# Optimization experiments

Measured on AMD Instinct MI355X. Metric: run time of the kernel, lower is better.

## Reference

```python
import jax, jax.numpy as jnp
import numpy as np

B, S, K, N = 4, 2048, 4096, 11008


def setup_inputs() -> dict:
    key = jax.random.key(0)
    k_x, k_w, k_s, k_z, k_b = jax.random.split(key, 5)
    x = jax.random.normal(k_x, (B, S, K), dtype=jnp.float32)
    qweight = jax.random.randint(k_w, (N, K), 0, 256, dtype=jnp.int32)
    scale = jax.random.uniform(k_s, (N, 1), dtype=jnp.float32) * 0.01 + 1e-4
    zero_point = jax.random.uniform(k_z, (N, 1), dtype=jnp.float32) * 255.0
    bias = jax.random.normal(k_b, (N,), dtype=jnp.float32)
    return {"x": x, "qweight": qweight, "scale": scale, "zero_point": zero_point, "bias": bias}


def reference(x, qweight, scale, zero_point, bias):
    # Dequantize int8 weights per output channel (group_size=-1):
    # w[n, k] = (qweight[n, k] - zero_point[n]) * scale[n]
    w = (qweight.astype(jnp.float32) - zero_point) * scale  # [N, K]
    # Fused dequant-matmul + bias: y = x @ w.T + b
    y = jnp.einsum('bsk,nk->bsn', x, w) + bias  # [B, S, N]
    return y
```

## Files before the change

### kernel.cpp

```cpp
#include <hip/hip_runtime.h>
#include <hip/hip_bf16.h>
#include <stdint.h>

#define M_DIM 8192
#define N_DIM 11008
#define K_DIM 4096
#define NTILE 64

typedef unsigned short ushort_t;
typedef __attribute__((ext_vector_type(8)))  short  short8;
typedef __attribute__((ext_vector_type(8)))  __bf16 bf16x8;
typedef __attribute__((ext_vector_type(4)))  float  f32x4;
typedef __attribute__((ext_vector_type(4)))  int    i32x4;
typedef __attribute__((ext_vector_type(16))) char   char16;

__device__ __forceinline__ ushort_t f2bf(float f){
  uint32_t u = __builtin_bit_cast(uint32_t, f);
  u += 0x7FFFu + ((u >> 16) & 1u);
  return (ushort_t)(u >> 16);
}

__device__ __forceinline__ void gll16(const void* g, void* l){
  __builtin_amdgcn_global_load_lds(
      (const __attribute__((address_space(1))) void*)g,
      (__attribute__((address_space(3))) void*)l,
      16, 0, 0);
}

__global__ __launch_bounds__(256)
void quant_x(const float* __restrict__ x, signed char* __restrict__ xq,
             float* __restrict__ sxv, float* __restrict__ sxs){
  const int row  = blockIdx.x;
  const int t    = threadIdx.x;
  const int lane = t & 63, wid = t >> 6;
  const float* xr = x + (size_t)row * K_DIM;

  float e[16];
  {
    const float4* p = (const float4*)(xr + t*16);
    float4 v0 = p[0], v1 = p[1], v2 = p[2], v3 = p[3];
    e[0]=v0.x; e[1]=v0.y; e[2]=v0.z; e[3]=v0.w;
    e[4]=v1.x; e[5]=v1.y; e[6]=v1.z; e[7]=v1.w;
    e[8]=v2.x; e[9]=v2.y; e[10]=v2.z; e[11]=v2.w;
    e[12]=v3.x; e[13]=v3.y; e[14]=v3.z; e[15]=v3.w;
  }
  float am = 0.f;
  #pragma unroll
  for (int j=0;j<16;++j) am = fmaxf(am, fabsf(e[j]));
  #pragma unroll
  for (int off=32; off; off>>=1) am = fmaxf(am, __shfl_xor(am, off));

  __shared__ float sm[4];
  __shared__ float ss[4];
  if (lane == 0) sm[wid] = am;
  __syncthreads();
  const float amax = fmaxf(fmaxf(sm[0],sm[1]), fmaxf(sm[2],sm[3]));
  const float inv = amax > 0.f ? 127.f/amax : 0.f;
  const float sx  = amax > 0.f ? amax*(1.f/127.f) : 1.f;

  char16 c;
  float fs = 0.f;
  #pragma unroll
  for (int j=0;j<16;++j){
    float r = rintf(e[j]*inv);
    fs += r;
    c[j] = (signed char)(int)r;
  }
  *(char16*)(xq + (size_t)row*K_DIM + t*16) = c;

  #pragma unroll
  for (int off=32; off; off>>=1) fs += __shfl_xor(fs, off);
  if (lane == 0) ss[wid] = fs;
  __syncthreads();
  if (t == 0){
    sxv[row] = sx;
    sxs[row] = ss[0]+ss[1]+ss[2]+ss[3];
  }
}

__global__ void cvt_w8(const int* __restrict__ q, signed char* __restrict__ wq){
  const int TOT = (int)((size_t)N_DIM*K_DIM/16);
  for (int c = blockIdx.x*blockDim.x + threadIdx.x; c < TOT; c += gridDim.x*blockDim.x){
    size_t i = (size_t)c*16;
    int4 a = *(const int4*)(q+i);
    int4 b = *(const int4*)(q+i+4);
    int4 d = *(const int4*)(q+i+8);
    int4 f = *(const int4*)(q+i+12);
    char16 o;
    o[0]=(signed char)(a.x-128);  o[1]=(signed char)(a.y-128);
    o[2]=(signed char)(a.z-128);  o[3]=(signed char)(a.w-128);
    o[4]=(signed char)(b.x-128);  o[5]=(signed char)(b.y-128);
    o[6]=(signed char)(b.z-128);  o[7]=(signed char)(b.w-128);
    o[8]=(signed char)(d.x-128);  o[9]=(signed char)(d.y-128);
    o[10]=(signed char)(d.z-128); o[11]=(signed char)(d.w-128);
    o[12]=(signed char)(f.x-128); o[13]=(signed char)(f.y-128);
    o[14]=(signed char)(f.z-128); o[15]=(signed char)(f.w-128);
    *(char16*)(wq+i) = o;
  }
}


#define BAR() do{ asm volatile("" ::: "memory"); \
  __builtin_amdgcn_s_barrier(); \
  asm volatile("" ::: "memory"); }while(0)

#define LGKM0() asm volatile("s_waitcnt lgkmcnt(0)" ::: "memory")

#define VMW2() do{ __builtin_amdgcn_sched_barrier(0); \
  asm volatile("s_waitcnt vmcnt(2)" ::: "memory"); \
  __builtin_amdgcn_sched_barrier(0); }while(0)

#define VMW0() do{ __builtin_amdgcn_sched_barrier(0); \
  asm volatile("s_waitcnt vmcnt(0)" ::: "memory"); \
  __builtin_amdgcn_sched_barrier(0); }while(0)

#define LDA_TO(DST, BUF, G) do{ \
  const signed char* _b = &As[BUF][wm][0]; \
  _Pragma("unroll") for (int mf=0; mf<4; ++mf) \
    DST[mf] = *(const i32x4*)(_b + ((G)*64 + mf*16 + rl)*64 + offk); \
}while(0)

#define LDB_TO(DST, BUF, NG) do{ \
  const signed char* _b = &Bs[BUF][hb][0]; \
  _Pragma("unroll") for (int nfl=0; nfl<2; ++nfl) \
    DST[nfl] = *(const i32x4*)(_b + (hbr + (NG)*32 + nfl*16 + rl)*64 + offk); \
}while(0)

#define MM_Q(AF, BF, MG, NG) do{ \
  __builtin_amdgcn_s_setprio(1); \
  _Pragma("unroll") for (int mf=0; mf<4; ++mf) \
    _Pragma("unroll") for (int nfl=0; nfl<2; ++nfl) \
      acc[(MG)*4+mf][(NG)*2+nfl] = __builtin_amdgcn_mfma_i32_16x16x64_i8( \
          AF[mf], BF[nfl], acc[(MG)*4+mf][(NG)*2+nfl], 0, 0, 0); \
  __builtin_amdgcn_s_setprio(0); \
}while(0)

#define STAGE_A(BUF, H, T) gll16(aS[H] + (size_t)(T)*64, &As[BUF][H][w*1024])
#define STAGE_B(BUF, H, T) gll16(bS[H] + (size_t)(T)*64, &Bs[BUF][H][w*1024])

__global__ __launch_bounds__(512, 1)
void qgemm256_i8(const signed char* __restrict__ Xq, const signed char* __restrict__ Wq,
                 const float* __restrict__ g_scale, const float* __restrict__ g_zp,
                 const float* __restrict__ g_bias,
                 const float* __restrict__ sxv, const float* __restrict__ sxs,
                 float* __restrict__ Y)
{
  __shared__ __align__(16) signed char As[2][2][8192];
  __shared__ __align__(16) signed char Bs[2][2][8192];

  const int t    = threadIdx.x;
  const int lane = t & 63;
  const int w    = t >> 6;
  const int wm   = w >> 2;
  const int wn   = w & 3;
  const int hb   = wn >> 1;
  const int hbr  = (wn & 1) * 64;

  const int GM2 = M_DIM/256, GN2 = N_DIM/256;
  const int NWG2 = GM2*GN2;
  int bid = blockIdx.x;
  int swz = (bid & 7) * (NWG2/8) + (bid >> 3);
  int by = swz / GN2, bx = swz - by*GN2;
  const int brow = by*256, bcol = bx*256;

  const int rl   = lane & 15;
  const int offk = ((lane >> 4) ^ ((rl >> 1) & 3)) * 16;

  const int g_s = (lane & 3) ^ ((lane >> 3) & 3);
  const signed char* aS[2];
  const signed char* bS[2];
  #pragma unroll
  for (int h=0; h<2; ++h){
    int r = h*128 + w*16 + (lane >> 2);
    aS[h] = Xq + (size_t)(brow + r)*K_DIM + g_s*16;
    bS[h] = Wq + (size_t)(bcol + r)*K_DIM + g_s*16;
  }

  i32x4 acc[8][4] = {};
  i32x4 afX[4], afY[4];
  i32x4 bfX[2], bfY[2];

  STAGE_B(0,0,0); STAGE_A(0,0,0); STAGE_A(0,1,0); STAGE_B(0,1,0);
  STAGE_B(1,0,1); STAGE_A(1,0,1);
  VMW2();
  BAR();

  #pragma unroll 1
  for (int j=0; j<NTILE/2-1; ++j){
    const int t1 = 2*j+1, t2 = 2*j+2, t3 = 2*j+3;
    LDA_TO(afX, 0, 0);
    LDB_TO(bfX, 0, 0);
    STAGE_A(1,1,t1);
    BAR(); LGKM0();
    MM_Q(afX, bfX, 0, 0);
    BAR();
    LDB_TO(bfY, 0, 1);
    STAGE_B(1,1,t1);
    BAR(); LGKM0();
    MM_Q(afX, bfY, 0, 1);
    BAR();
    LDA_TO(afY, 0, 1);
    STAGE_B(0,0,t2);
    BAR(); LGKM0();
    MM_Q(afY, bfX, 1, 0);
    BAR();
    STAGE_A(0,0,t2);
    VMW2();
    BAR();
    MM_Q(afY, bfY, 1, 1);
    BAR();
    LDA_TO(afX, 1, 0);
    LDB_TO(bfX, 1, 0);
    STAGE_A(0,1,t2);
    BAR(); LGKM0();
    MM_Q(afX, bfX, 0, 0);
    BAR();
    LDB_TO(bfY, 1, 1);
    STAGE_B(0,1,t2);
    BAR(); LGKM0();
    MM_Q(afX, bfY, 0, 1);
    BAR();
    LDA_TO(afY, 1, 1);
    STAGE_B(1,0,t3);
    BAR(); LGKM0();
    MM_Q(afY, bfX, 1, 0);
    BAR();
    STAGE_A(1,0,t3);
    VMW2();
    BAR();
    MM_Q(afY, bfY, 1, 1);
    BAR();
  }

  {
    const int t1 = NTILE-1;
    LDA_TO(afX, 0, 0);
    LDB_TO(bfX, 0, 0);
    STAGE_A(1,1,t1);
    BAR(); LGKM0();
    MM_Q(afX, bfX, 0, 0);
    BAR();
    LDB_TO(bfY, 0, 1);
    STAGE_B(1,1,t1);
    BAR(); LGKM0();
    MM_Q(afX, bfY, 0, 1);
    BAR();
    LDA_TO(afY, 0, 1);
    BAR(); LGKM0();
    MM_Q(afY, bfX, 1, 0);
    BAR();
    VMW0();
    BAR();
    MM_Q(afY, bfY, 1, 1);
    BAR();
    LDA_TO(afX, 1, 0);
    LDB_TO(bfX, 1, 0);
    BAR(); LGKM0();
    MM_Q(afX, bfX, 0, 0);
    BAR();
    LDB_TO(bfY, 1, 1);
    BAR(); LGKM0();
    MM_Q(afX, bfY, 0, 1);
    BAR();
    LDA_TO(afY, 1, 1);
    BAR(); LGKM0();
    MM_Q(afY, bfX, 1, 0);
    BAR();
    MM_Q(afY, bfY, 1, 1);
  }

  const int cl = lane & 15;
  const int rq = (lane >> 4) << 2;
  float sN[4], cN[4], bN[4];
  #pragma unroll
  for (int nf=0; nf<4; ++nf){
    int col = bcol + wn*64 + nf*16 + cl;
    float s = g_scale[col];
    sN[nf] = s;
    cN[nf] = s * (128.f - g_zp[col]);
    bN[nf] = g_bias[col];
  }
  #pragma unroll
  for (int mf=0; mf<8; ++mf){
    const int rowb = brow + wm*128 + mf*16 + rq;
    float sx0 = sxv[rowb],   sx1 = sxv[rowb+1], sx2 = sxv[rowb+2], sx3 = sxv[rowb+3];
    float t0 = sx0*sxs[rowb],   t1 = sx1*sxs[rowb+1];
    float t2 = sx2*sxs[rowb+2], t3 = sx3*sxs[rowb+3];
    #pragma unroll
    for (int nf=0; nf<4; ++nf){
      int col = bcol + wn*64 + nf*16 + cl;
      size_t base = (size_t)rowb*N_DIM + col;
      i32x4 v = acc[mf][nf];
      Y[base            ] = (float)v[0]*(sN[nf]*sx0) + t0*cN[nf] + bN[nf];
      Y[base +   N_DIM  ] = (float)v[1]*(sN[nf]*sx1) + t1*cN[nf] + bN[nf];
      Y[base + 2*N_DIM  ] = (float)v[2]*(sN[nf]*sx2) + t2*cN[nf] + bN[nf];
      Y[base + 3*N_DIM  ] = (float)v[3]*(sN[nf]*sx3) + t3*cN[nf] + bN[nf];
    }
  }
}

__global__ __launch_bounds__(256, 2)
void qgemm_fb(const float* __restrict__ Xf, const int* __restrict__ Wq,
              const float* __restrict__ g_scale, const float* __restrict__ g_zp,
              const float* __restrict__ g_bias, float* __restrict__ Y)
{
  const int BM=128, BK=64, NT=K_DIM/BK, GRID_N=N_DIM/128, NWG=(M_DIM/128)*GRID_N;
  __shared__ __align__(16) ushort_t As[2][BM*BK];
  __shared__ __align__(16) ushort_t Bs[2][BM*BK];

  const int t = threadIdx.x, lane = t & 63, w = t >> 6;
  const int wr = w >> 1, wc = w & 1;
  int bid = blockIdx.x;
  int swz = (bid & 7) * (NWG/8) + (bid >> 3);
  int by = swz / GRID_N, bx = swz - by*GRID_N;
  const int brow = by*128, bcol = bx*128;

  f32x4 acc[4][4] = {};
  const int s8 = t & 7, r0 = t >> 3;

  float wsc[4], wof[4];
  #pragma unroll
  for (int i=0;i<4;++i){
    int n = bcol + r0 + 32*i;
    float sc = g_scale[n];
    wsc[i] = sc; wof[i] = -g_zp[n]*sc;
  }
  float4 ax[4][2]; int4 bq[4][2];
  auto loadA = [&](int kt){
    #pragma unroll
    for (int i=0;i<4;++i){
      const float* p = Xf + (size_t)(brow + r0 + 32*i)*K_DIM + kt*BK + s8*8;
      ax[i][0] = *(const float4*)p; ax[i][1] = *(const float4*)(p+4);
    }};
  auto loadB = [&](int kt){
    #pragma unroll
    for (int i=0;i<4;++i){
      const int* p = Wq + (size_t)(bcol + r0 + 32*i)*K_DIM + kt*BK + s8*8;
      bq[i][0] = *(const int4*)p; bq[i][1] = *(const int4*)(p+4);
    }};
  auto stageA = [&](int buf){
    #pragma unroll
    for (int i=0;i<4;++i){
      short8 o;
      o[0]=(short)f2bf(ax[i][0].x); o[1]=(short)f2bf(ax[i][0].y);
      o[2]=(short)f2bf(ax[i][0].z); o[3]=(short)f2bf(ax[i][0].w);
      o[4]=(short)f2bf(ax[i][1].x); o[5]=(short)f2bf(ax[i][1].y);
      o[6]=(short)f2bf(ax[i][1].z); o[7]=(short)f2bf(ax[i][1].w);
      int r = r0 + 32*i; int idx = (r*BK + s8*8) ^ ((r&7)<<3);
      *(short8*)&As[buf][idx] = o; }};
  auto stageB = [&](int buf){
    #pragma unroll
    for (int i=0;i<4;++i){
      short8 o;
      o[0]=(short)f2bf((float)bq[i][0].x*wsc[i]+wof[i]);
      o[1]=(short)f2bf((float)bq[i][0].y*wsc[i]+wof[i]);
      o[2]=(short)f2bf((float)bq[i][0].z*wsc[i]+wof[i]);
      o[3]=(short)f2bf((float)bq[i][0].w*wsc[i]+wof[i]);
      o[4]=(short)f2bf((float)bq[i][1].x*wsc[i]+wof[i]);
      o[5]=(short)f2bf((float)bq[i][1].y*wsc[i]+wof[i]);
      o[6]=(short)f2bf((float)bq[i][1].z*wsc[i]+wof[i]);
      o[7]=(short)f2bf((float)bq[i][1].w*wsc[i]+wof[i]);
      int r = r0 + 32*i; int idx = (r*BK + s8*8) ^ ((r&7)<<3);
      *(short8*)&Bs[buf][idx] = o; }};

  loadA(0); loadB(0);
  stageA(0); stageB(0);
  if (NT > 1){ loadA(1); loadB(1); }

  int cur = 0;
  for (int kt=0; kt<NT; ++kt){
    asm volatile("s_waitcnt vmcnt(0) lgkmcnt(0)" ::: "memory");
    __builtin_amdgcn_sched_barrier(0);
    __syncthreads();
    const int nxt = cur ^ 1;
    if (kt+1 < NT){
      stageA(nxt); stageB(nxt);
      if (kt+2 < NT){ loadA(kt+2); loadB(kt+2); }
    }
    const ushort_t* as = As[cur];
    const ushort_t* bs = Bs[cur];
    #pragma unroll
    for (int kk=0; kk<2; ++kk){
      bf16x8 af[4], bfr[4];
      const int klo = kk*32 + ((lane>>4)<<3);
      #pragma unroll
      for (int mf=0; mf<4; ++mf){
        int r = wr*64 + mf*16 + (lane&15);
        af[mf] = *(const bf16x8*)&as[(r*BK + klo) ^ ((r&7)<<3)];
      }
      #pragma unroll
      for (int nf=0; nf<4; ++nf){
        int r = wc*64 + nf*16 + (lane&15);
        bfr[nf] = *(const bf16x8*)&bs[(r*BK + klo) ^ ((r&7)<<3)];
      }
      #pragma unroll
      for (int mf=0; mf<4; ++mf)
        #pragma unroll
        for (int nf=0; nf<4; ++nf)
          acc[mf][nf] = __builtin_amdgcn_mfma_f32_16x16x32_bf16(af[mf], bfr[nf], acc[mf][nf], 0,0,0);
    }
    cur = nxt;
  }
  const int cl = lane & 15, rq = (lane >> 4) << 2;
  #pragma unroll
  for (int nf=0; nf<4; ++nf){
    int col = bcol + wc*64 + nf*16 + cl;
    float bvs = g_bias[col];
    #pragma unroll
    for (int mf=0; mf<4; ++mf){
      int row = brow + wr*64 + mf*16 + rq;
      f32x4 v = acc[mf][nf];
      #pragma unroll
      for (int i=0;i<4;++i)
        Y[(size_t)(row+i)*N_DIM + col] = v[i] + bvs;
    }
  }
}

extern "C" void kernel_launch(void* const* d_in, const int* in_sizes, int n_in,
                              void* d_out, int out_size, void* d_ws, size_t ws_size,
                              hipStream_t stream) {
  const float* x     = (const float*)d_in[0];
  const int*   qw    = (const int*)  d_in[1];
  const float* scale = (const float*)d_in[2];
  const float* zp    = (const float*)d_in[3];
  const float* bias  = (const float*)d_in[4];
  float* y = (float*)d_out;

  const size_t XQ = (size_t)M_DIM*K_DIM;
  const size_t WQ = (size_t)N_DIM*K_DIM;
  const size_t SV = (size_t)M_DIM*4;
  const size_t need = XQ + WQ + 2*SV;

  if (ws_size >= need){
    signed char* xq = (signed char*)d_ws;
    signed char* wq = (signed char*)d_ws + XQ;
    float* sxv = (float*)((char*)d_ws + XQ + WQ);
    float* sxs = sxv + M_DIM;
    quant_x<<<dim3(M_DIM), dim3(256), 0, stream>>>(x, xq, sxv, sxs);
    cvt_w8<<<dim3(2048), dim3(256), 0, stream>>>(qw, wq);
    qgemm256_i8<<<dim3((M_DIM/256)*(N_DIM/256)), dim3(512), 0, stream>>>(
        xq, wq, scale, zp, bias, sxv, sxs, y);
  } else {
    qgemm_fb<<<dim3((M_DIM/128)*(N_DIM/128)), dim3(256), 0, stream>>>(
        x, qw, scale, zp, bias, y);
  }
}
```

Before: 572.3 us.

## Prefetch LDS fragments one phase ahead with partial lgkmcnt waits

```diff
diff --git a/kernel.cpp b/kernel.cpp
--- a/kernel.cpp
+++ b/kernel.cpp
@@ -104,7 +104,9 @@
   __builtin_amdgcn_s_barrier(); \
   asm volatile("" ::: "memory"); }while(0)
 
-#define LGKM0() asm volatile("s_waitcnt lgkmcnt(0)" ::: "memory")
+#define LGKMW(N) do{ \
+  asm volatile("s_waitcnt lgkmcnt(" #N ")" ::: "memory"); \
+  __builtin_amdgcn_sched_barrier(0); }while(0)
 
 #define VMW2() do{ __builtin_amdgcn_sched_barrier(0); \
   asm volatile("s_waitcnt vmcnt(2)" ::: "memory"); \
@@ -184,88 +186,104 @@
   STAGE_B(1,0,1); STAGE_A(1,0,1);
   VMW2();
   BAR();
+  LDA_TO(afX, 0, 0);
+  LDB_TO(bfX, 0, 0);
 
   #pragma unroll 1
   for (int j=0; j<NTILE/2-1; ++j){
     const int t1 = 2*j+1, t2 = 2*j+2, t3 = 2*j+3;
+    LDB_TO(bfY, 0, 1);
+    STAGE_A(1,1,t1);
+    BAR();
+    LGKMW(2);
+    MM_Q(afX, bfX, 0, 0);
+    BAR();
+    LDA_TO(afY, 0, 1);
+    STAGE_B(1,1,t1);
+    BAR();
+    LGKMW(4);
+    MM_Q(afX, bfY, 0, 1);
+    BAR();
+    STAGE_B(0,0,t2);
+    BAR();
+    LGKMW(0);
+    MM_Q(afY, bfX, 1, 0);
+    BAR();
+    STAGE_A(0,0,t2);
+    VMW2();
+    BAR();
+    LDA_TO(afX, 1, 0);
+    LDB_TO(bfX, 1, 0);
+    LGKMW(6);
+    MM_Q(afY, bfY, 1, 1);
+    BAR();
+    LDB_TO(bfY, 1, 1);
+    STAGE_A(0,1,t2);
+    BAR();
+    LGKMW(2);
+    MM_Q(afX, bfX, 0, 0);
+    BAR();
+    LDA_TO(afY, 1, 1);
+    STAGE_B(0,1,t2);
+    BAR();
+    LGKMW(4);
+    MM_Q(afX, bfY, 0, 1);
+    BAR();
+    STAGE_B(1,0,t3);
+    BAR();
+    LGKMW(0);
+    MM_Q(afY, bfX, 1, 0);
+    BAR();
+    STAGE_A(1,0,t3);
+    VMW2();
+    BAR();
     LDA_TO(afX, 0, 0);
     LDB_TO(bfX, 0, 0);
+    LGKMW(6);
+    MM_Q(afY, bfY, 1, 1);
+    BAR();
+  }
+
+  {
+    const int t1 = NTILE-1;
+    LDB_TO(bfY, 0, 1);
     STAGE_A(1,1,t1);
-    BAR(); LGKM0();
+    BAR();
+    LGKMW(2);
     MM_Q(afX, bfX, 0, 0);
     BAR();
-    LDB_TO(bfY, 0, 1);
+    LDA_TO(afY, 0, 1);
     STAGE_B(1,1,t1);
-    BAR(); LGKM0();
+    BAR();
+    LGKMW(4);
     MM_Q(afX, bfY, 0, 1);
     BAR();
-    LDA_TO(afY, 0, 1);
-    STAGE_B(0,0,t2);
-    BAR(); LGKM0();
+    BAR();
+    LGKMW(0);
     MM_Q(afY, bfX, 1, 0);
     BAR();
-    STAGE_A(0,0,t2);
-    VMW2();
-    BAR();
-    MM_Q(afY, bfY, 1, 1);
+    VMW0();
     BAR();
     LDA_TO(afX, 1, 0);
     LDB_TO(bfX, 1, 0);
-    STAGE_A(0,1,t2);
-    BAR(); LGKM0();
+    LGKMW(6);
+    MM_Q(afY, bfY, 1, 1);
+    BAR();
+    LDB_TO(bfY, 1, 1);
+    BAR();
+    LGKMW(2);
     MM_Q(afX, bfX, 0, 0);
     BAR();
-    LDB_TO(bfY, 1, 1);
-    STAGE_B(0,1,t2);
-    BAR(); LGKM0();
+    LDA_TO(afY, 1, 1);
+    BAR();
+    LGKMW(4);
     MM_Q(afX, bfY, 0, 1);
     BAR();
-    LDA_TO(afY, 1, 1);
-    STAGE_B(1,0,t3);
-    BAR(); LGKM0();
+    BAR();
+    LGKMW(0);
     MM_Q(afY, bfX, 1, 0);
     BAR();
-    STAGE_A(1,0,t3);
-    VMW2();
-    BAR();
-    MM_Q(afY, bfY, 1, 1);
-    BAR();
-  }
-
-  {
-    const int t1 = NTILE-1;
-    LDA_TO(afX, 0, 0);
-    LDB_TO(bfX, 0, 0);
-    STAGE_A(1,1,t1);
-    BAR(); LGKM0();
-    MM_Q(afX, bfX, 0, 0);
-    BAR();
-    LDB_TO(bfY, 0, 1);
-    STAGE_B(1,1,t1);
-    BAR(); LGKM0();
-    MM_Q(afX, bfY, 0, 1);
-    BAR();
-    LDA_TO(afY, 0, 1);
-    BAR(); LGKM0();
-    MM_Q(afY, bfX, 1, 0);
-    BAR();
-    VMW0();
-    BAR();
-    MM_Q(afY, bfY, 1, 1);
-    BAR();
-    LDA_TO(afX, 1, 0);
-    LDB_TO(bfX, 1, 0);
-    BAR(); LGKM0();
-    MM_Q(afX, bfX, 0, 0);
-    BAR();
-    LDB_TO(bfY, 1, 1);
-    BAR(); LGKM0();
-    MM_Q(afX, bfY, 0, 1);
-    BAR();
-    LDA_TO(afY, 1, 1);
-    BAR(); LGKM0();
-    MM_Q(afY, bfX, 1, 0);
-    BAR();
+    LGKMW(0);
     MM_Q(afY, bfY, 1, 1);
   }
 
```

After: 570.0 us. Within noise of the previous version (-0.4%).
